# Optimization experiments

Hardware: AMD Instinct MI355X
Metric: run time of the kernel (lower is better)

## Reference

```python
import jax, jax.numpy as jnp
import numpy as np

N_NODES = 200000
N_EDGES = 3200000
N_GRAPHS = 64
IN_DIM, HIDDEN, OUT_DIM = 128, 16, 64


def setup_inputs() -> dict:
    key = jax.random.key(0)
    ks = jax.random.split(key, 5)
    x = jax.random.normal(ks[0], (N_NODES, IN_DIM), dtype=jnp.float32)
    edge_index = jax.random.randint(ks[1], (2, N_EDGES), 0, N_NODES, dtype=jnp.int64)
    batch = jnp.sort(jax.random.randint(ks[2], (N_NODES,), 0, N_GRAPHS, dtype=jnp.int64))
    W1 = jax.random.normal(ks[3], (IN_DIM, HIDDEN), dtype=jnp.float32) * (1.0 / np.sqrt(IN_DIM))
    W2 = jax.random.normal(ks[4], (HIDDEN, OUT_DIM), dtype=jnp.float32) * (1.0 / np.sqrt(HIDDEN))
    b1 = jnp.zeros((HIDDEN,), jnp.float32)
    b2 = jnp.zeros((OUT_DIM,), jnp.float32)
    return {"x": x, "edge_index": edge_index, "batch": batch,
            "W1": W1, "b1": b1, "W2": W2, "b2": b2, "training": 0}


def _gcn_conv(x, W, b, row, col, n_nodes):
    # PyG GCNConv: add-self-loop symmetric normalization, transform then
    # gather-from-row / scatter-add-to-col.  (row, col) already include self-loops.
    h = x @ W                                             # [N, out]
    deg = jnp.zeros((n_nodes,), h.dtype).at[col].add(1.0)  # degree incl. self-loop (>=1)
    dinv = deg ** -0.5
    norm = dinv[row] * dinv[col]                          # [E+N]
    out = jnp.zeros((n_nodes, W.shape[1]), h.dtype).at[col].add(h[row] * norm[:, None])
    return out + b


def reference(x, edge_index, batch, W1, b1, W2, b2, training):
    n = x.shape[0]
    loops = jnp.arange(n, dtype=edge_index.dtype)
    row = jnp.concatenate([edge_index[0], loops])
    col = jnp.concatenate([edge_index[1], loops])
    h = _gcn_conv(x, W1, b1, row, col, n)
    h = jax.nn.relu(h)
    # F.dropout with training=False is identity (reference is deterministic)
    h = _gcn_conv(h, W2, b2, row, col, n)
    # per-graph sum pooling: replaces the Python torch.where loop
    graph_embeds = jax.ops.segment_sum(h, batch, num_segments=N_GRAPHS)
    return graph_embeds
```

## Files before the change

### kernel.cpp

```cpp
#include <hip/hip_runtime.h>


#define TPB 256
#define CHUNK 4096
#define BK_SHIFT 9
#define NPB 512

__device__ __forceinline__ float bf2f(unsigned short u) {
    union { unsigned int i; float f; } v; v.i = ((unsigned int)u) << 16; return v.f;
}
__device__ __forceinline__ unsigned short f2bf(float f) {
    union { float f; unsigned int i; } v; v.f = f;
    unsigned int r = v.i + 0x7fff + ((v.i >> 16) & 1);
    return (unsigned short)(r >> 16);
}

__global__ __launch_bounds__(TPB) void hist_kernel(const int* __restrict__ col,
                                                   int* __restrict__ counts,
                                                   int E, int nblk, int nbuck) {
    __shared__ int hist[512];
    int t = threadIdx.x;
    for (int i = t; i < nbuck; i += TPB) hist[i] = 0;
    __syncthreads();
    int e0 = blockIdx.x * CHUNK;
    for (int i = t; i < CHUNK; i += TPB) {
        int e = e0 + i;
        if (e < E) atomicAdd(&hist[col[e] >> BK_SHIFT], 1);
    }
    __syncthreads();
    for (int i = t; i < nbuck; i += TPB) counts[i * nblk + blockIdx.x] = hist[i];
}

__global__ __launch_bounds__(TPB) void scan1_kernel(const int* __restrict__ in,
                                                    int* __restrict__ out,
                                                    int* __restrict__ bsum, int L) {
    __shared__ int s[TPB];
    int t = threadIdx.x;
    int i = blockIdx.x * TPB + t;
    int d = (i < L) ? in[i] : 0;
    s[t] = d; __syncthreads();
    for (int off = 1; off < TPB; off <<= 1) {
        int v = (t >= off) ? s[t - off] : 0;
        __syncthreads();
        s[t] += v;
        __syncthreads();
    }
    if (i < L) out[i] = s[t] - d;
    if (t == TPB - 1) bsum[blockIdx.x] = s[t];
}

__global__ __launch_bounds__(1024) void scan2_kernel(int* __restrict__ bsum, int nb) {
    __shared__ int s[1024];
    int t = threadIdx.x;
    int i0 = t * 2, i1 = t * 2 + 1;
    int v0 = (i0 < nb) ? bsum[i0] : 0;
    int v1 = (i1 < nb) ? bsum[i1] : 0;
    int pv = v0 + v1;
    s[t] = pv; __syncthreads();
    for (int off = 1; off < 1024; off <<= 1) {
        int u = (t >= off) ? s[t - off] : 0;
        __syncthreads();
        s[t] += u;
        __syncthreads();
    }
    int exc = s[t] - pv;
    if (i0 < nb) bsum[i0] = exc;
    if (i1 < nb) bsum[i1] = exc + v0;
}

__device__ __forceinline__ int cbase_at(const int* counts, const int* bsum, int f) {
    return counts[f] + bsum[f >> 8];
}

__global__ __launch_bounds__(TPB) void s1c_gemm_kernel(
        const int* __restrict__ row, const int* __restrict__ col,
        const int* __restrict__ counts, const int* __restrict__ bsum,
        int E, int nblk, int nbuck,
        int* __restrict__ bucketed,
        const float* __restrict__ x, const float* __restrict__ W1,
        unsigned short* __restrict__ h1b, int N, int nbg) {
    __shared__ int cur[NPB];
    __shared__ float w1s[128 * 16];
    int b = (int)blockIdx.x, t = threadIdx.x;
    int M = min(nblk, nbg);
    int role, id;
    if (b < 2 * M) { role = b & 1; id = b >> 1; }
    else           { role = (nblk > nbg) ? 0 : 1; id = b - M; }

    if (role == 0) {
        for (int i = t; i < nbuck; i += TPB)
            cur[i] = cbase_at(counts, bsum, i * nblk + id);
        __syncthreads();
        int e0 = id * CHUNK;
        for (int i = t; i < CHUNK; i += TPB) {
            int e = e0 + i;
            if (e < E) {
                int c = col[e];
                int pos = atomicAdd(&cur[c >> BK_SHIFT], 1);
                bucketed[pos] = ((c & (NPB - 1)) << 18) | row[e];
            }
        }
        return;
    }
    for (int i = t; i < 128 * 16; i += TPB) w1s[i] = W1[i];
    __syncthreads();
    int n = id * TPB + t;
    if (n >= N) return;
    const float4* xr = (const float4*)(x + (size_t)n * 128);
    float acc[16];
#pragma unroll
    for (int k = 0; k < 16; ++k) acc[k] = 0.f;
#pragma unroll 1
    for (int g = 0; g < 8; ++g) {
        float4 v0 = xr[g * 4 + 0], v1 = xr[g * 4 + 1];
        float4 v2 = xr[g * 4 + 2], v3 = xr[g * 4 + 3];
        float xv[16] = {v0.x, v0.y, v0.z, v0.w, v1.x, v1.y, v1.z, v1.w,
                        v2.x, v2.y, v2.z, v2.w, v3.x, v3.y, v3.z, v3.w};
#pragma unroll
        for (int cc = 0; cc < 16; ++cc) {
            const float4* w4 = (const float4*)&w1s[(g * 16 + cc) * 16];
            float4 wa = w4[0], wb = w4[1], wc = w4[2], wd = w4[3];
            float xc = xv[cc];
            acc[0]  = fmaf(xc, wa.x, acc[0]);  acc[1]  = fmaf(xc, wa.y, acc[1]);
            acc[2]  = fmaf(xc, wa.z, acc[2]);  acc[3]  = fmaf(xc, wa.w, acc[3]);
            acc[4]  = fmaf(xc, wb.x, acc[4]);  acc[5]  = fmaf(xc, wb.y, acc[5]);
            acc[6]  = fmaf(xc, wb.z, acc[6]);  acc[7]  = fmaf(xc, wb.w, acc[7]);
            acc[8]  = fmaf(xc, wc.x, acc[8]);  acc[9]  = fmaf(xc, wc.y, acc[9]);
            acc[10] = fmaf(xc, wc.z, acc[10]); acc[11] = fmaf(xc, wc.w, acc[11]);
            acc[12] = fmaf(xc, wd.x, acc[12]); acc[13] = fmaf(xc, wd.y, acc[13]);
            acc[14] = fmaf(xc, wd.z, acc[14]); acc[15] = fmaf(xc, wd.w, acc[15]);
        }
    }
    unsigned int u[8];
#pragma unroll
    for (int j = 0; j < 8; ++j)
        u[j] = (unsigned int)f2bf(acc[2 * j]) | ((unsigned int)f2bf(acc[2 * j + 1]) << 16);
    uint4* o = (uint4*)(h1b + (size_t)n * 16);
    o[0] = make_uint4(u[0], u[1], u[2], u[3]);
    o[1] = make_uint4(u[4], u[5], u[6], u[7]);
}

__global__ __launch_bounds__(TPB) void sort_kernel(
        const int* __restrict__ bucketed,
        const int* __restrict__ counts, const int* __restrict__ bsum,
        int E, int nblk, int nbuck,
        int* __restrict__ csr, int* __restrict__ offs, float* __restrict__ dinv,
        const unsigned short* __restrict__ h1b, unsigned short* __restrict__ h1p, int N) {
    __shared__ int lhist[NPB];
    __shared__ int part[TPB];
    __shared__ float sdinv[NPB];
    int bk = blockIdx.x, t = threadIdx.x;
    int n0 = bk << BK_SHIFT;
    int n1 = min(n0 + NPB, N);
    int e0 = cbase_at(counts, bsum, bk * nblk);
    int e1 = (bk + 1 < nbuck) ? cbase_at(counts, bsum, (bk + 1) * nblk) : E;

    lhist[t] = 0; lhist[t + TPB] = 0;
    __syncthreads();
    for (int i = e0 + t; i < e1; i += TPB)
        atomicAdd(&lhist[bucketed[i] >> 18], 1);
    __syncthreads();

    int base = t * 2;
    int c0 = lhist[base], c1 = lhist[base + 1];
    int s = c0 + c1;
    part[t] = s;
    __syncthreads();
    for (int off = 1; off < TPB; off <<= 1) {
        int v = (t >= off) ? part[t - off] : 0;
        __syncthreads();
        part[t] += v;
        __syncthreads();
    }
    int o0 = e0 + part[t] - s;
    int o1 = o0 + c0;
    lhist[base] = o0; lhist[base + 1] = o1;
    sdinv[base]     = rsqrtf((float)c0 + 1.0f);
    sdinv[base + 1] = rsqrtf((float)c1 + 1.0f);
    int n = n0 + base;
    if (n + 0 < N) { offs[n + 0] = o0; dinv[n + 0] = sdinv[base]; }
    if (n + 1 < N) { offs[n + 1] = o1; dinv[n + 1] = sdinv[base + 1]; }
    __syncthreads();

    for (int i = e0 + t; i < e1; i += TPB) {
        int v = bucketed[i];
        int pos = atomicAdd(&lhist[v >> 18], 1);
        csr[pos] = v & 0x3FFFF;
    }
    int nq = (n1 - n0) * 4;
    for (int i = t; i < nq; i += TPB) {
        float dv = sdinv[i >> 2];
        uint2 u = ((const uint2*)h1b)[(size_t)n0 * 4 + i];
        float f0 = bf2f((unsigned short)(u.x & 0xffff));
        float f1 = bf2f((unsigned short)(u.x >> 16));
        float f2 = bf2f((unsigned short)(u.y & 0xffff));
        float f3 = bf2f((unsigned short)(u.y >> 16));
        ((ushort4*)h1p)[(size_t)n0 * 4 + i] =
            make_ushort4(f2bf(f0 * dv), f2bf(f1 * dv), f2bf(f2 * dv), f2bf(f3 * dv));
    }
    if (bk == 0 && t == 0) offs[N] = E;
}

__global__ __launch_bounds__(TPB) void gather1_kernel(const int* __restrict__ csr,
                                                      const int* __restrict__ offs,
                                                      const unsigned short* __restrict__ h1p,
                                                      const float* __restrict__ dinv,
                                                      const float* __restrict__ b1,
                                                      unsigned short* __restrict__ h2p, int N) {
    int t = threadIdx.x;
    int c = blockIdx.x * 16 + (t >> 4);
    int k = t & 15;
    if (c >= N) return;
    int p0 = offs[c], p1 = offs[c + 1];
    float acc = 0.f;
    for (int p = p0; p < p1; p += 32) {
        int s0 = csr[min(p + k, p1 - 1)];
        int s1 = csr[min(p + 16 + k, p1 - 1)];
        int rem = p1 - p;
        float v[32];
#pragma unroll
        for (int j = 0; j < 16; ++j) {
            int sj = __shfl(s0, j, 16);
            v[j] = bf2f(h1p[(size_t)sj * 16 + k]);
        }
#pragma unroll
        for (int j = 0; j < 16; ++j) {
            int sj = __shfl(s1, j, 16);
            v[16 + j] = bf2f(h1p[(size_t)sj * 16 + k]);
        }
#pragma unroll
        for (int j = 0; j < 32; ++j) acc += (j < rem) ? v[j] : 0.f;
    }
    float dc = dinv[c];
    float self = bf2f(h1p[(size_t)c * 16 + k]);
    float a = fmaf(dc, acc + self, b1[k]);
    h2p[(size_t)c * 16 + k] = f2bf(dc * fmaxf(a, 0.f));
}

__global__ __launch_bounds__(TPB) void gather2f_kernel(
        const int* __restrict__ csr, const int* __restrict__ offs,
        const unsigned short* __restrict__ h2p, const float* __restrict__ dinv,
        const float* __restrict__ W2, const float* __restrict__ b2,
        const int* __restrict__ batch, float* __restrict__ out, int N) {
    __shared__ float w2s[16 * 64];
    __shared__ float asT[64 * 17];
    __shared__ float pool[64];
    int t = threadIdx.x;
    for (int i = t; i < 16 * 64; i += TPB) w2s[i] = W2[i];
    if (t < 64) pool[t] = 0.f;

    int n0 = blockIdx.x * 64;
    int nLast = min(n0 + 63, N - 1);
    int g0 = batch[n0];
    bool uniform = (batch[nLast] == g0);

    int grp = t >> 4, k = t & 15;
#pragma unroll 1
    for (int it = 0; it < 4; ++it) {
        int m = grp * 4 + it;
        int c = n0 + m;
        if (c < N) {
            int p0 = offs[c], p1 = offs[c + 1];
            float acc = 0.f;
            for (int p = p0; p < p1; p += 32) {
                int s0 = csr[min(p + k, p1 - 1)];
                int s1 = csr[min(p + 16 + k, p1 - 1)];
                int rem = p1 - p;
                float v[32];
#pragma unroll
                for (int j = 0; j < 16; ++j) {
                    int sj = __shfl(s0, j, 16);
                    v[j] = bf2f(h2p[(size_t)sj * 16 + k]);
                }
#pragma unroll
                for (int j = 0; j < 16; ++j) {
                    int sj = __shfl(s1, j, 16);
                    v[16 + j] = bf2f(h2p[(size_t)sj * 16 + k]);
                }
#pragma unroll
                for (int j = 0; j < 32; ++j) acc += (j < rem) ? v[j] : 0.f;
            }
            float self = bf2f(h2p[(size_t)c * 16 + k]);
            asT[m * 17 + k] = dinv[c] * (acc + self);
        }
    }
    __syncthreads();

    int wave = t >> 6, j = t & 63;
    float w2reg[16];
#pragma unroll
    for (int kk = 0; kk < 16; ++kk) w2reg[kk] = w2s[kk * 64 + j];
    float b2j = b2[j];
    float val = 0.f;
    int g_cur = -1;
#pragma unroll 1
    for (int mi = 0; mi < 16; ++mi) {
        int m = wave * 16 + mi;
        int c = n0 + m;
        if (c >= N) break;
        const float* ar = &asT[m * 17];
        float y = b2j;
#pragma unroll
        for (int kk = 0; kk < 16; ++kk) y = fmaf(ar[kk], w2reg[kk], y);
        if (uniform) {
            val += y;
        } else {
            int g = batch[c];
            if (g != g_cur) {
                if (g_cur >= 0) atomicAdd(&out[(size_t)g_cur * 64 + j], val);
                val = 0.f;
                g_cur = g;
            }
            val += y;
        }
    }
    if (uniform) {
        atomicAdd(&pool[j], val);
        __syncthreads();
        if (t < 64) atomicAdd(&out[(size_t)g0 * 64 + t], pool[t]);
    } else {
        if (g_cur >= 0) atomicAdd(&out[(size_t)g_cur * 64 + j], val);
    }
}

static inline size_t align64(size_t v) { return (v + 63) & ~(size_t)63; }

extern "C" void kernel_launch(void* const* d_in, const int* in_sizes, int n_in,
                              void* d_out, int out_size, void* d_ws, size_t ws_size,
                              hipStream_t stream) {
    const float* x     = (const float*)d_in[0];
    const int*   ei    = (const int*)d_in[1];
    const int*   batch = (const int*)d_in[2];
    const float* W1    = (const float*)d_in[3];
    const float* b1    = (const float*)d_in[4];
    const float* W2    = (const float*)d_in[5];
    const float* b2    = (const float*)d_in[6];

    const int N = in_sizes[0] / 128;
    const int E = in_sizes[1] / 2;
    const int* row = ei;
    const int* col = ei + E;

    const int NBLK  = (E + CHUNK - 1) / CHUNK;
    const int NBUCK = (N + NPB - 1) / NPB;
    const int L     = NBUCK * NBLK;
    const int NBS   = (L + TPB - 1) / TPB;
    const int NBG   = (N + TPB - 1) / TPB;

    char* p = (char*)d_ws;
    int*            counts   = (int*)p;            p += align64((size_t)L * 4);
    int*            bsum     = (int*)p;            p += align64(2048 * 4);
    int*            bucketed = (int*)p;            p += align64((size_t)E * 4);
    int*            csr      = (int*)p;            p += align64((size_t)E * 4);
    int*            offs     = (int*)p;            p += align64((size_t)(N + 1) * 4);
    float*          dinv     = (float*)p;          p += align64((size_t)N * 4);
    unsigned short* h1b      = (unsigned short*)p; p += align64((size_t)N * 16 * 2);
    unsigned short* h1p      = (unsigned short*)p; p += align64((size_t)N * 16 * 2);
    unsigned short* h2p      = (unsigned short*)p; p += align64((size_t)N * 16 * 2);
    float*          out      = (float*)d_out;

    hipMemsetAsync(out, 0, (size_t)out_size * sizeof(float), stream);

    hist_kernel<<<NBLK, TPB, 0, stream>>>(col, counts, E, NBLK, NBUCK);
    scan1_kernel<<<NBS, TPB, 0, stream>>>(counts, counts, bsum, L);
    scan2_kernel<<<1, 1024, 0, stream>>>(bsum, NBS);
    s1c_gemm_kernel<<<NBLK + NBG, TPB, 0, stream>>>(row, col, counts, bsum,
                                                    E, NBLK, NBUCK,
                                                    bucketed, x, W1, h1b, N, NBG);
    sort_kernel<<<NBUCK, TPB, 0, stream>>>(bucketed, counts, bsum, E, NBLK, NBUCK,
                                           csr, offs, dinv, h1b, h1p, N);
    gather1_kernel<<<(N + 15) / 16, TPB, 0, stream>>>(csr, offs, h1p, dinv, b1, h2p, N);
    gather2f_kernel<<<(N + 63) / 64, TPB, 0, stream>>>(csr, offs, h2p, dinv,
                                                       W2, b2, batch, out, N);
}
```

Before: 359.0 us.

## Replace CSR sort with per-bucket shared-memory atomic aggregation over bucketed edges

Removes the within-bucket counting sort that built a CSR array and offsets. Each 256-node bucket block instead scans its bucketed edges and accumulates neighbor features into a shared-memory tile with atomic adds, for both GCN layers. Bucket size is halved so the tile fits, and the scan is widened to handle the larger number of block sums. This drops the CSR write and reread, at the cost of heavy LDS atomic contention and a fixed 256-node-per-block parallelism.

```diff
diff --git a/kernel.cpp b/kernel.cpp
--- a/kernel.cpp
+++ b/kernel.cpp
@@ -3,8 +3,8 @@
 
 #define TPB 256
 #define CHUNK 4096
-#define BK_SHIFT 9
-#define NPB 512
+#define BK_SHIFT 8
+#define NPB 256
 
 __device__ __forceinline__ float bf2f(unsigned short u) {
     union { unsigned int i; float f; } v; v.i = ((unsigned int)u) << 16; return v.f;
@@ -18,7 +18,7 @@
 __global__ __launch_bounds__(TPB) void hist_kernel(const int* __restrict__ col,
                                                    int* __restrict__ counts,
                                                    int E, int nblk, int nbuck) {
-    __shared__ int hist[512];
+    __shared__ int hist[1024];
     int t = threadIdx.x;
     for (int i = t; i < nbuck; i += TPB) hist[i] = 0;
     __syncthreads();
@@ -31,13 +31,12 @@
     for (int i = t; i < nbuck; i += TPB) counts[i * nblk + blockIdx.x] = hist[i];
 }
 
-__global__ __launch_bounds__(TPB) void scan1_kernel(const int* __restrict__ in,
-                                                    int* __restrict__ out,
+__global__ __launch_bounds__(TPB) void scan1_kernel(int* __restrict__ counts,
                                                     int* __restrict__ bsum, int L) {
     __shared__ int s[TPB];
     int t = threadIdx.x;
     int i = blockIdx.x * TPB + t;
-    int d = (i < L) ? in[i] : 0;
+    int d = (i < L) ? counts[i] : 0;
     s[t] = d; __syncthreads();
     for (int off = 1; off < TPB; off <<= 1) {
         int v = (t >= off) ? s[t - off] : 0;
@@ -45,17 +44,20 @@
         s[t] += v;
         __syncthreads();
     }
-    if (i < L) out[i] = s[t] - d;
+    if (i < L) counts[i] = s[t] - d;
     if (t == TPB - 1) bsum[blockIdx.x] = s[t];
 }
 
 __global__ __launch_bounds__(1024) void scan2_kernel(int* __restrict__ bsum, int nb) {
     __shared__ int s[1024];
     int t = threadIdx.x;
-    int i0 = t * 2, i1 = t * 2 + 1;
-    int v0 = (i0 < nb) ? bsum[i0] : 0;
-    int v1 = (i1 < nb) ? bsum[i1] : 0;
-    int pv = v0 + v1;
+    int base = t * 4;
+    int v[4], pv = 0;
+#pragma unroll
+    for (int u = 0; u < 4; ++u) {
+        v[u] = (base + u < nb) ? bsum[base + u] : 0;
+        pv += v[u];
+    }
     s[t] = pv; __syncthreads();
     for (int off = 1; off < 1024; off <<= 1) {
         int u = (t >= off) ? s[t - off] : 0;
@@ -64,8 +66,11 @@
         __syncthreads();
     }
     int exc = s[t] - pv;
-    if (i0 < nb) bsum[i0] = exc;
-    if (i1 < nb) bsum[i1] = exc + v0;
+#pragma unroll
+    for (int u = 0; u < 4; ++u) {
+        if (base + u < nb) bsum[base + u] = exc;
+        exc += v[u];
+    }
 }
 
 __device__ __forceinline__ int cbase_at(const int* counts, const int* bsum, int f) {
@@ -79,7 +84,7 @@
         int* __restrict__ bucketed,
         const float* __restrict__ x, const float* __restrict__ W1,
         unsigned short* __restrict__ h1b, int N, int nbg) {
-    __shared__ int cur[NPB];
+    __shared__ int cur[1024];
     __shared__ float w1s[128 * 16];
     int b = (int)blockIdx.x, t = threadIdx.x;
     int M = min(nblk, nbg);
@@ -140,172 +145,167 @@
     o[1] = make_uint4(u[4], u[5], u[6], u[7]);
 }
 
-__global__ __launch_bounds__(TPB) void sort_kernel(
+__global__ __launch_bounds__(TPB) void degscale_kernel(
         const int* __restrict__ bucketed,
         const int* __restrict__ counts, const int* __restrict__ bsum,
         int E, int nblk, int nbuck,
-        int* __restrict__ csr, int* __restrict__ offs, float* __restrict__ dinv,
+        float* __restrict__ dinv,
         const unsigned short* __restrict__ h1b, unsigned short* __restrict__ h1p, int N) {
     __shared__ int lhist[NPB];
-    __shared__ int part[TPB];
     __shared__ float sdinv[NPB];
     int bk = blockIdx.x, t = threadIdx.x;
     int n0 = bk << BK_SHIFT;
-    int n1 = min(n0 + NPB, N);
+    int nn = min(NPB, N - n0);
     int e0 = cbase_at(counts, bsum, bk * nblk);
     int e1 = (bk + 1 < nbuck) ? cbase_at(counts, bsum, (bk + 1) * nblk) : E;
 
-    lhist[t] = 0; lhist[t + TPB] = 0;
+    lhist[t] = 0;
     __syncthreads();
     for (int i = e0 + t; i < e1; i += TPB)
         atomicAdd(&lhist[bucketed[i] >> 18], 1);
     __syncthreads();
-
-    int base = t * 2;
-    int c0 = lhist[base], c1 = lhist[base + 1];
-    int s = c0 + c1;
-    part[t] = s;
-    __syncthreads();
-    for (int off = 1; off < TPB; off <<= 1) {
-        int v = (t >= off) ? part[t - off] : 0;
-        __syncthreads();
-        part[t] += v;
-        __syncthreads();
-    }
-    int o0 = e0 + part[t] - s;
-    int o1 = o0 + c0;
-    lhist[base] = o0; lhist[base + 1] = o1;
-    sdinv[base]     = rsqrtf((float)c0 + 1.0f);
-    sdinv[base + 1] = rsqrtf((float)c1 + 1.0f);
-    int n = n0 + base;
-    if (n + 0 < N) { offs[n + 0] = o0; dinv[n + 0] = sdinv[base]; }
-    if (n + 1 < N) { offs[n + 1] = o1; dinv[n + 1] = sdinv[base + 1]; }
-    __syncthreads();
-
-    for (int i = e0 + t; i < e1; i += TPB) {
-        int v = bucketed[i];
-        int pos = atomicAdd(&lhist[v >> 18], 1);
-        csr[pos] = v & 0x3FFFF;
-    }
-    int nq = (n1 - n0) * 4;
-    for (int i = t; i < nq; i += TPB) {
-        float dv = sdinv[i >> 2];
-        uint2 u = ((const uint2*)h1b)[(size_t)n0 * 4 + i];
-        float f0 = bf2f((unsigned short)(u.x & 0xffff));
-        float f1 = bf2f((unsigned short)(u.x >> 16));
-        float f2 = bf2f((unsigned short)(u.y & 0xffff));
-        float f3 = bf2f((unsigned short)(u.y >> 16));
-        ((ushort4*)h1p)[(size_t)n0 * 4 + i] =
-            make_ushort4(f2bf(f0 * dv), f2bf(f1 * dv), f2bf(f2 * dv), f2bf(f3 * dv));
-    }
-    if (bk == 0 && t == 0) offs[N] = E;
-}
-
-__global__ __launch_bounds__(TPB) void gather1_kernel(const int* __restrict__ csr,
-                                                      const int* __restrict__ offs,
-                                                      const unsigned short* __restrict__ h1p,
-                                                      const float* __restrict__ dinv,
-                                                      const float* __restrict__ b1,
-                                                      unsigned short* __restrict__ h2p, int N) {
-    int t = threadIdx.x;
-    int c = blockIdx.x * 16 + (t >> 4);
-    int k = t & 15;
-    if (c >= N) return;
-    int p0 = offs[c], p1 = offs[c + 1];
-    float acc = 0.f;
-    for (int p = p0; p < p1; p += 32) {
-        int s0 = csr[min(p + k, p1 - 1)];
-        int s1 = csr[min(p + 16 + k, p1 - 1)];
-        int rem = p1 - p;
-        float v[32];
-#pragma unroll
-        for (int j = 0; j < 16; ++j) {
-            int sj = __shfl(s0, j, 16);
-            v[j] = bf2f(h1p[(size_t)sj * 16 + k]);
-        }
-#pragma unroll
-        for (int j = 0; j < 16; ++j) {
-            int sj = __shfl(s1, j, 16);
-            v[16 + j] = bf2f(h1p[(size_t)sj * 16 + k]);
-        }
-#pragma unroll
-        for (int j = 0; j < 32; ++j) acc += (j < rem) ? v[j] : 0.f;
-    }
-    float dc = dinv[c];
-    float self = bf2f(h1p[(size_t)c * 16 + k]);
-    float a = fmaf(dc, acc + self, b1[k]);
-    h2p[(size_t)c * 16 + k] = f2bf(dc * fmaxf(a, 0.f));
-}
-
-__global__ __launch_bounds__(TPB) void gather2f_kernel(
-        const int* __restrict__ csr, const int* __restrict__ offs,
+    float dv = rsqrtf((float)lhist[t] + 1.0f);
+    sdinv[t] = dv;
+    if (t < nn) dinv[n0 + t] = dv;
+    __syncthreads();
+
+    const uint2* src = (const uint2*)h1b;
+    uint2* dst = (uint2*)h1p;
+    for (int i = t; i < nn * 4; i += TPB) {
+        float d = sdinv[i >> 2];
+        uint2 u = src[(size_t)n0 * 4 + i];
+        float f0 = bf2f((unsigned short)(u.x & 0xffff)) * d;
+        float f1 = bf2f((unsigned short)(u.x >> 16)) * d;
+        float f2 = bf2f((unsigned short)(u.y & 0xffff)) * d;
+        float f3 = bf2f((unsigned short)(u.y >> 16)) * d;
+        uint2 w;
+        w.x = (unsigned int)f2bf(f0) | ((unsigned int)f2bf(f1) << 16);
+        w.y = (unsigned int)f2bf(f2) | ((unsigned int)f2bf(f3) << 16);
+        dst[(size_t)n0 * 4 + i] = w;
+    }
+}
+
+__device__ __forceinline__ void agg_edges(const int* __restrict__ bucketed,
+                                          const unsigned short* __restrict__ h,
+                                          float* acc, int e0, int e1, int t) {
+    int h2 = t & 1;
+    for (int i0 = e0 + (t >> 1); i0 < e1; i0 += 512) {
+        int ent[4]; uint4 val[4]; bool ok[4];
+#pragma unroll
+        for (int u = 0; u < 4; ++u) {
+            int i = i0 + u * 128;
+            ok[u] = i < e1;
+            ent[u] = bucketed[ok[u] ? i : e0];
+        }
+#pragma unroll
+        for (int u = 0; u < 4; ++u) {
+            int src = ent[u] & 0x3FFFF;
+            val[u] = ((const uint4*)h)[(size_t)src * 2 + h2];
+        }
+#pragma unroll
+        for (int u = 0; u < 4; ++u) {
+            if (ok[u]) {
+                float* a = &acc[(ent[u] >> 18) * 17 + h2 * 8];
+                atomicAdd(a + 0, bf2f((unsigned short)(val[u].x & 0xffff)));
+                atomicAdd(a + 1, bf2f((unsigned short)(val[u].x >> 16)));
+                atomicAdd(a + 2, bf2f((unsigned short)(val[u].y & 0xffff)));
+                atomicAdd(a + 3, bf2f((unsigned short)(val[u].y >> 16)));
+                atomicAdd(a + 4, bf2f((unsigned short)(val[u].z & 0xffff)));
+                atomicAdd(a + 5, bf2f((unsigned short)(val[u].z >> 16)));
+                atomicAdd(a + 6, bf2f((unsigned short)(val[u].w & 0xffff)));
+                atomicAdd(a + 7, bf2f((unsigned short)(val[u].w >> 16)));
+            }
+        }
+    }
+}
+
+__global__ __launch_bounds__(TPB) void agg1_kernel(
+        const int* __restrict__ bucketed,
+        const int* __restrict__ counts, const int* __restrict__ bsum,
+        int E, int nblk, int nbuck,
+        const unsigned short* __restrict__ h1p, const float* __restrict__ dinv,
+        const float* __restrict__ b1, unsigned short* __restrict__ h2p, int N) {
+    __shared__ float acc[NPB * 17];
+    int bk = blockIdx.x, t = threadIdx.x;
+    int n0 = bk << BK_SHIFT;
+    int nn = min(NPB, N - n0);
+    int e0 = cbase_at(counts, bsum, bk * nblk);
+    int e1 = (bk + 1 < nbuck) ? cbase_at(counts, bsum, (bk + 1) * nblk) : E;
+
+    for (int i = t; i < NPB * 17; i += TPB) acc[i] = 0.f;
+    __syncthreads();
+    agg_edges(bucketed, h1p, acc, e0, e1, t);
+    __syncthreads();
+
+    for (int i = t; i < nn * 8; i += TPB) {
+        int m = i >> 3, q = i & 7;
+        int c = n0 + m;
+        float dc = dinv[c];
+        unsigned int us = *(const unsigned int*)&h1p[(size_t)c * 16 + 2 * q];
+        float a0 = acc[m * 17 + 2 * q]     + bf2f((unsigned short)(us & 0xffff));
+        float a1 = acc[m * 17 + 2 * q + 1] + bf2f((unsigned short)(us >> 16));
+        float r0 = dc * fmaxf(fmaf(dc, a0, b1[2 * q]), 0.f);
+        float r1 = dc * fmaxf(fmaf(dc, a1, b1[2 * q + 1]), 0.f);
+        *(unsigned int*)&h2p[(size_t)c * 16 + 2 * q] =
+            (unsigned int)f2bf(r0) | ((unsigned int)f2bf(r1) << 16);
+    }
+}
+
+__global__ __launch_bounds__(TPB) void agg2f_kernel(
+        const int* __restrict__ bucketed,
+        const int* __restrict__ counts, const int* __restrict__ bsum,
+        int E, int nblk, int nbuck,
         const unsigned short* __restrict__ h2p, const float* __restrict__ dinv,
         const float* __restrict__ W2, const float* __restrict__ b2,
         const int* __restrict__ batch, float* __restrict__ out, int N) {
+    __shared__ float acc[NPB * 17];
     __shared__ float w2s[16 * 64];
-    __shared__ float asT[64 * 17];
     __shared__ float pool[64];
-    int t = threadIdx.x;
+    int bk = blockIdx.x, t = threadIdx.x;
+    int n0 = bk << BK_SHIFT;
+    int nn = min(NPB, N - n0);
+    int e0 = cbase_at(counts, bsum, bk * nblk);
+    int e1 = (bk + 1 < nbuck) ? cbase_at(counts, bsum, (bk + 1) * nblk) : E;
+
+    for (int i = t; i < NPB * 17; i += TPB) acc[i] = 0.f;
     for (int i = t; i < 16 * 64; i += TPB) w2s[i] = W2[i];
     if (t < 64) pool[t] = 0.f;
-
-    int n0 = blockIdx.x * 64;
-    int nLast = min(n0 + 63, N - 1);
-    int g0 = batch[n0];
-    bool uniform = (batch[nLast] == g0);
-
-    int grp = t >> 4, k = t & 15;
-#pragma unroll 1
-    for (int it = 0; it < 4; ++it) {
-        int m = grp * 4 + it;
+    __syncthreads();
+    agg_edges(bucketed, h2p, acc, e0, e1, t);
+    __syncthreads();
+
+    for (int i = t; i < nn * 8; i += TPB) {
+        int m = i >> 3, q = i & 7;
         int c = n0 + m;
-        if (c < N) {
-            int p0 = offs[c], p1 = offs[c + 1];
-            float acc = 0.f;
-            for (int p = p0; p < p1; p += 32) {
-                int s0 = csr[min(p + k, p1 - 1)];
-                int s1 = csr[min(p + 16 + k, p1 - 1)];
-                int rem = p1 - p;
-                float v[32];
-#pragma unroll
-                for (int j = 0; j < 16; ++j) {
-                    int sj = __shfl(s0, j, 16);
-                    v[j] = bf2f(h2p[(size_t)sj * 16 + k]);
-                }
-#pragma unroll
-                for (int j = 0; j < 16; ++j) {
-                    int sj = __shfl(s1, j, 16);
-                    v[16 + j] = bf2f(h2p[(size_t)sj * 16 + k]);
-                }
-#pragma unroll
-                for (int j = 0; j < 32; ++j) acc += (j < rem) ? v[j] : 0.f;
-            }
-            float self = bf2f(h2p[(size_t)c * 16 + k]);
-            asT[m * 17 + k] = dinv[c] * (acc + self);
-        }
+        float dc = dinv[c];
+        unsigned int us = *(const unsigned int*)&h2p[(size_t)c * 16 + 2 * q];
+        acc[m * 17 + 2 * q]     = dc * (acc[m * 17 + 2 * q]     + bf2f((unsigned short)(us & 0xffff)));
+        acc[m * 17 + 2 * q + 1] = dc * (acc[m * 17 + 2 * q + 1] + bf2f((unsigned short)(us >> 16)));
     }
     __syncthreads();
 
     int wave = t >> 6, j = t & 63;
     float w2reg[16];
 #pragma unroll
-    for (int kk = 0; kk < 16; ++kk) w2reg[kk] = w2s[kk * 64 + j];
+    for (int k = 0; k < 16; ++k) w2reg[k] = w2s[k * 64 + j];
     float b2j = b2[j];
+    int g0 = batch[n0];
+    bool uniform = (batch[min(n0 + NPB - 1, N - 1)] == g0);
+
     float val = 0.f;
     int g_cur = -1;
 #pragma unroll 1
-    for (int mi = 0; mi < 16; ++mi) {
-        int m = wave * 16 + mi;
-        int c = n0 + m;
-        if (c >= N) break;
-        const float* ar = &asT[m * 17];
+    for (int mi = 0; mi < 64; ++mi) {
+        int m = wave * 64 + mi;
+        if (m >= nn) break;
+        const float* ar = &acc[m * 17];
         float y = b2j;
 #pragma unroll
-        for (int kk = 0; kk < 16; ++kk) y = fmaf(ar[kk], w2reg[kk], y);
+        for (int k = 0; k < 16; ++k) y = fmaf(ar[k], w2reg[k], y);
         if (uniform) {
             val += y;
         } else {
-            int g = batch[c];
+            int g = batch[n0 + m];
             if (g != g_cur) {
                 if (g_cur >= 0) atomicAdd(&out[(size_t)g_cur * 64 + j], val);
                 val = 0.f;
@@ -349,10 +349,8 @@
 
     char* p = (char*)d_ws;
     int*            counts   = (int*)p;            p += align64((size_t)L * 4);
-    int*            bsum     = (int*)p;            p += align64(2048 * 4);
+    int*            bsum     = (int*)p;            p += align64(4096 * 4);
     int*            bucketed = (int*)p;            p += align64((size_t)E * 4);
-    int*            csr      = (int*)p;            p += align64((size_t)E * 4);
-    int*            offs     = (int*)p;            p += align64((size_t)(N + 1) * 4);
     float*          dinv     = (float*)p;          p += align64((size_t)N * 4);
     unsigned short* h1b      = (unsigned short*)p; p += align64((size_t)N * 16 * 2);
     unsigned short* h1p      = (unsigned short*)p; p += align64((size_t)N * 16 * 2);
@@ -362,14 +360,15 @@
     hipMemsetAsync(out, 0, (size_t)out_size * sizeof(float), stream);
 
     hist_kernel<<<NBLK, TPB, 0, stream>>>(col, counts, E, NBLK, NBUCK);
-    scan1_kernel<<<NBS, TPB, 0, stream>>>(counts, counts, bsum, L);
+    scan1_kernel<<<NBS, TPB, 0, stream>>>(counts, bsum, L);
     scan2_kernel<<<1, 1024, 0, stream>>>(bsum, NBS);
     s1c_gemm_kernel<<<NBLK + NBG, TPB, 0, stream>>>(row, col, counts, bsum,
                                                     E, NBLK, NBUCK,
                                                     bucketed, x, W1, h1b, N, NBG);
-    sort_kernel<<<NBUCK, TPB, 0, stream>>>(bucketed, counts, bsum, E, NBLK, NBUCK,
-                                           csr, offs, dinv, h1b, h1p, N);
-    gather1_kernel<<<(N + 15) / 16, TPB, 0, stream>>>(csr, offs, h1p, dinv, b1, h2p, N);
-    gather2f_kernel<<<(N + 63) / 64, TPB, 0, stream>>>(csr, offs, h2p, dinv,
-                                                       W2, b2, batch, out, N);
-}
+    degscale_kernel<<<NBUCK, TPB, 0, stream>>>(bucketed, counts, bsum, E, NBLK, NBUCK,
+                                               dinv, h1b, h1p, N);
+    agg1_kernel<<<NBUCK, TPB, 0, stream>>>(bucketed, counts, bsum, E, NBLK, NBUCK,
+                                           h1p, dinv, b1, h2p, N);
+    agg2f_kernel<<<NBUCK, TPB, 0, stream>>>(bucketed, counts, bsum, E, NBLK, NBUCK,
+                                            h2p, dinv, W2, b2, batch, out, N);
+}
```

Measured after the change: 963.9 us. 168% more time.
